# Optimization experiments

Measured on AMD Instinct MI355X. Metric: run time of the kernel, lower is better.

Reference implementation:

```python
import jax, jax.numpy as jnp
import numpy as np

NEG_SLOPE = 0.2  # PyG GATConv default negative_slope


def gat_conv(x, src, dst, W, a_src, a_dst, b, N):
    """Single PyG-style GATConv (add_self_loops already applied via src/dst).
    x: [N, F_in], W: [F_in, H*C], a_src/a_dst: [H, C], b: [H*C].
    Returns [N, H*C] (concat=True)."""
    H, C = a_src.shape
    h = (x @ W).reshape(N, H, C)                      # [N,H,C]
    alpha_src = jnp.sum(h * a_src[None], axis=-1)      # [N,H]
    alpha_dst = jnp.sum(h * a_dst[None], axis=-1)      # [N,H]
    e = jax.nn.leaky_relu(alpha_src[src] + alpha_dst[dst], NEG_SLOPE)  # [E,H]
    # numerically stable segment softmax over incoming edges of each dst node
    m = jax.ops.segment_max(e, dst, num_segments=N)    # [N,H]
    m = jnp.where(jnp.isfinite(m), m, 0.0)
    ex = jnp.exp(e - m[dst])                           # [E,H]
    den = jax.ops.segment_sum(ex, dst, num_segments=N) # [N,H]
    alpha = ex / (den[dst] + 1e-16)                    # [E,H]
    out = jax.ops.segment_sum(h[src] * alpha[..., None], dst, num_segments=N)  # [N,H,C]
    return out.reshape(N, H * C) + b


def setup_inputs() -> dict:
    key = jax.random.key(0)
    ks = jax.random.split(key, 9)
    B, N, E = 2, 50000, 800000
    d_model, n_hidden, en_dim, H = 128, 128, 64, 1
    fea_mats = jax.random.normal(ks[0], (B, N, d_model), dtype=jnp.float32)
    edge_index = jax.random.randint(ks[1], (B, 2, E), 0, N, dtype=jnp.int32)
    s1 = 1.0 / np.sqrt(d_model)
    s2 = 1.0 / np.sqrt(n_hidden)
    return {
        "fea_mats": fea_mats,
        "edge_index": edge_index,
        "W1": jax.random.normal(ks[2], (d_model, H * n_hidden), dtype=jnp.float32) * s1,
        "att_src1": jax.random.normal(ks[3], (H, n_hidden), dtype=jnp.float32) * s2,
        "att_dst1": jax.random.normal(ks[4], (H, n_hidden), dtype=jnp.float32) * s2,
        "b1": jnp.zeros((H * n_hidden,), dtype=jnp.float32),
        "W2": jax.random.normal(ks[5], (H * n_hidden, H * en_dim), dtype=jnp.float32) * s2,
        "att_src2": jax.random.normal(ks[6], (H, en_dim), dtype=jnp.float32) / np.sqrt(en_dim),
        "att_dst2": jax.random.normal(ks[7], (H, en_dim), dtype=jnp.float32) / np.sqrt(en_dim),
        "b2": jnp.zeros((H * en_dim,), dtype=jnp.float32),
    }


def reference(fea_mats, edge_index, W1, att_src1, att_dst1, b1, W2, att_src2, att_dst2, b2):
    B, N, _ = fea_mats.shape
    loops = jnp.arange(N, dtype=edge_index.dtype)

    def per_graph(x, ei):
        # PyG GATConv adds self-loops by default
        src = jnp.concatenate([ei[0], loops])
        dst = jnp.concatenate([ei[1], loops])
        h = gat_conv(x, src, dst, W1, att_src1, att_dst1, b1, N)
        h = jax.nn.relu(h)
        h = gat_conv(h, src, dst, W2, att_src2, att_dst2, b2, N)
        return h  # [N, en_dim]

    return jax.vmap(per_graph)(fea_mats, edge_index)  # [B, N, en_dim]
```

## Files before the change

kernel.cpp:

```cpp
#include <hip/hip_runtime.h>

#define NEG_SLOPE 0.2f
static constexpr int BLK = 256;
static constexpr int EPB = 4096;
static constexpr int CAP = 6144;

typedef short bf16x8 __attribute__((ext_vector_type(8)));
typedef float f32x4  __attribute__((ext_vector_type(4)));
typedef unsigned short u16x8 __attribute__((ext_vector_type(8)));
typedef unsigned short u16x4 __attribute__((ext_vector_type(4)));

static inline int cdiv(long a, long b){ return (int)((a + b - 1) / b); }

__device__ __forceinline__ unsigned short f2bf(float f){
    unsigned u = __float_as_uint(f);
    u += 0x7fff + ((u >> 16) & 1);
    return (unsigned short)(u >> 16);
}
__device__ __forceinline__ float bf2f(unsigned short h){
    return __uint_as_float(((unsigned)h) << 16);
}
__device__ __forceinline__ float lrelu(float v){
    return v > 0.f ? v : NEG_SLOPE * v;
}

struct GP {
    const int* src; const int* dst; const float* X;
    int* gcnt; int* gbase; int* ebuf; int* rowptr; int* csrsrc;
    unsigned short* h1b; unsigned short* h2b;
    float *as1, *ad1, *as2, *ad2; float* outp;
};

template<int CO, int CT, bool RELU_IN, bool BF16OUT>
__device__ __forceinline__ void gemm_dev(
    int bid, const float* __restrict__ X,
    const unsigned short* __restrict__ Wt_hi, const unsigned short* __restrict__ Wt_lo,
    const float* __restrict__ avs, const float* __restrict__ avd,
    void* __restrict__ Hout, float* __restrict__ as_out, float* __restrict__ ad_out,
    int N, unsigned short* smem)
{
    constexpr int CHUNKS = CO / (CT * 16);
    constexpr int HWB = CT * 4096;
    int ch, rtb;
    if (CHUNKS == 1){ ch = 0; rtb = bid; } else { ch = bid & 1; rtb = bid >> 1; }
    int c0 = ch * (CT * 16);

    {
        const char* srch = (const char*)(Wt_hi + (size_t)c0 * 128);
        const char* srcl = (const char*)(Wt_lo + (size_t)c0 * 128);
        #pragma unroll
        for (int it = 0; it < CT * 2; ++it){
            int o = (it * 256 + (int)threadIdx.x) * 16;
            const char* sp = (o < HWB) ? (srch + o) : (srcl + (o - HWB));
            u16x8 v = *(const u16x8*)sp;
            int so = o ^ (((o >> 8) & 7) << 4);
            *(u16x8*)((char*)smem + so) = v;
        }
    }
    __syncthreads();

    int wave = threadIdx.x >> 6;
    int lane = threadIdx.x & 63;
    int RTt = N >> 4;
    int rt0 = rtb * 8 + wave;
    int rt1 = rt0 + 4;
    if (rt0 >= RTt) return;
    bool vB = rt1 < RTt;
    int rl = lane & 15, g = lane >> 4;
    const float* xrowA = X + (long)(rt0 * 16 + rl) * 128 + g * 8;
    const float* xrowB = X + (long)((vB ? rt1 : rt0) * 16 + rl) * 128 + g * 8;

    f32x4 accA[CT], accB[CT];
    #pragma unroll
    for (int t = 0; t < CT; t++){ accA[t] = (f32x4)(0.f); accB[t] = (f32x4)(0.f); }

    int sw = (rl & 7) << 4;
    #pragma unroll
    for (int ks = 0; ks < 4; ks++){
        float4 xaA = *(const float4*)(xrowA + ks * 32);
        float4 xbA = *(const float4*)(xrowA + ks * 32 + 4);
        float4 xaB = *(const float4*)(xrowB + ks * 32);
        float4 xbB = *(const float4*)(xrowB + ks * 32 + 4);
        float xvA[8] = {xaA.x, xaA.y, xaA.z, xaA.w, xbA.x, xbA.y, xbA.z, xbA.w};
        float xvB[8] = {xaB.x, xaB.y, xaB.z, xaB.w, xbB.x, xbB.y, xbB.z, xbB.w};
        bf16x8 xbfA, xbfB;
        #pragma unroll
        for (int j = 0; j < 8; j++){
            float xA = xvA[j], xB = xvB[j];
            if (RELU_IN){ xA = fmaxf(xA, 0.f); xB = fmaxf(xB, 0.f); }
            xbfA[j] = (short)f2bf(xA);
            xbfB[j] = (short)f2bf(xB);
        }
        int rbase = rl * 256 + ks * 64 + g * 16;
        #pragma unroll
        for (int t = 0; t < CT; t++){
            bf16x8 wh = *(const bf16x8*)((char*)smem + ((t * 4096 + rbase) ^ sw));
            bf16x8 wl = *(const bf16x8*)((char*)smem + ((HWB + t * 4096 + rbase) ^ sw));
            accA[t] = __builtin_amdgcn_mfma_f32_16x16x32_bf16(wh, xbfA, accA[t], 0, 0, 0);
            accB[t] = __builtin_amdgcn_mfma_f32_16x16x32_bf16(wh, xbfB, accB[t], 0, 0, 0);
            accA[t] = __builtin_amdgcn_mfma_f32_16x16x32_bf16(wl, xbfA, accA[t], 0, 0, 0);
            accB[t] = __builtin_amdgcn_mfma_f32_16x16x32_bf16(wl, xbfB, accB[t], 0, 0, 0);
        }
    }

    #pragma unroll
    for (int half = 0; half < 2; half++){
        if (half == 1 && !vB) break;
        int r0 = (half == 0 ? rt0 : rt1) << 4;
        f32x4* acc = (half == 0) ? accA : accB;
        float ps = 0.f, pd = 0.f;
        #pragma unroll
        for (int t = 0; t < CT; t++){
            int c = c0 + t * 16 + 4 * g;
            float4 vs4 = *(const float4*)(avs + c);
            float4 vd4 = *(const float4*)(avd + c);
            ps += acc[t][0]*vs4.x + acc[t][1]*vs4.y + acc[t][2]*vs4.z + acc[t][3]*vs4.w;
            pd += acc[t][0]*vd4.x + acc[t][1]*vd4.y + acc[t][2]*vd4.z + acc[t][3]*vd4.w;
            long base = (long)(r0 + rl) * CO + c;
            if (BF16OUT){
                u16x4 pk;
                #pragma unroll
                for (int r = 0; r < 4; r++) pk[r] = f2bf(acc[t][r]);
                *(u16x4*)((unsigned short*)Hout + base) = pk;
            } else {
                float4 pv;
                pv.x = acc[t][0]; pv.y = acc[t][1]; pv.z = acc[t][2]; pv.w = acc[t][3];
                *(float4*)((float*)Hout + base) = pv;
            }
        }
        ps += __shfl_xor(ps, 16, 64); ps += __shfl_xor(ps, 32, 64);
        pd += __shfl_xor(pd, 16, 64); pd += __shfl_xor(pd, 32, 64);
        if (g == 0){
            unsafeAtomicAdd(as_out + r0 + rl, ps);
            unsafeAtomicAdd(ad_out + r0 + rl, pd);
        }
    }
}

__device__ __forceinline__ void bucket_dev(
    int bid, const GP* __restrict__ g, int E, int Etot, int nbk, unsigned short* smem)
{
    int* spk   = (int*)smem;
    int* shist = spk + 4096;
    int* sbase = shist + 256;
    int tid = (int)threadIdx.x;
    for (int i = tid; i < nbk; i += 256) shist[i] = 0;
    __syncthreads();
    int e0 = bid * EPB;
    #pragma unroll
    for (int i = 0; i < EPB / 256; i++){
        int idx = i * 256 + tid; int e = e0 + idx;
        unsigned p = 0xFFFFFFFFu;
        if (e < Etot){
            int s, d;
            if (e < E){ s = g->src[e]; d = g->dst[e]; } else { s = e - E; d = s; }
            p = ((unsigned)s << 16) | (unsigned)d;
            atomicAdd(&shist[d >> 8], 1);
        }
        spk[idx] = (int)p;
    }
    __syncthreads();
    for (int i = tid; i < nbk; i += 256){
        sbase[i] = atomicAdd(&g->gcnt[i], shist[i]);
        shist[i] = 0;
    }
    __syncthreads();
    #pragma unroll
    for (int i = 0; i < EPB / 256; i++){
        int idx = i * 256 + tid;
        unsigned p = (unsigned)spk[idx];
        if (p != 0xFFFFFFFFu){
            int d = (int)(p & 0xFFFFu); int b = d >> 8;
            int r = sbase[b] + atomicAdd(&shist[b], 1);
            if (r < CAP) g->ebuf[(size_t)b * CAP + r] = (int)p;
        }
    }
}

__device__ __forceinline__ void fine_dev(int k, const GP* __restrict__ g, int N, int Etot)
{
    __shared__ int pk2[CAP];
    __shared__ int fs[256];
    __shared__ int fill[256];
    __shared__ int fh[256];
    int tid = (int)threadIdx.x;
    int cnt = min(g->gcnt[k], CAP);
    int bb  = g->gbase[k];
    for (int i = tid; i < cnt; i += 256) pk2[i] = g->ebuf[(size_t)k * CAP + i];
    fh[tid] = 0; fill[tid] = 0;
    __syncthreads();
    for (int i = tid; i < cnt; i += 256) atomicAdd(&fh[pk2[i] & 255], 1);
    __syncthreads();
    int v = fh[tid];
    fs[tid] = v;
    __syncthreads();
    #pragma unroll
    for (int off = 1; off < 256; off <<= 1){
        int t = (tid >= off) ? fs[tid - off] : 0;
        __syncthreads();
        fs[tid] += t;
        __syncthreads();
    }
    int excl = fs[tid] - v;
    __syncthreads();
    fs[tid] = excl;
    __syncthreads();
    int node = k * 256 + tid;
    if (node < N) g->rowptr[node] = bb + excl;
    if (k == 0 && tid == 0) g->rowptr[N] = Etot;
    for (int i = tid; i < cnt; i += 256){
        unsigned p = (unsigned)pk2[i];
        int f = (int)(p & 255u);
        int r = atomicAdd(&fill[f], 1);
        g->csrsrc[bb + fs[f] + r] = (int)(p >> 16);
    }
}

template<int CO, int GRP>
__device__ __forceinline__ void agg_core(
    const int* __restrict__ rowptr, const int* __restrict__ csr_src,
    const float* __restrict__ as, const float* __restrict__ ad,
    const unsigned short* __restrict__ hb, int node, int ql, float* acc)
{
    int start = rowptr[node];
    int deg   = rowptr[node + 1] - start;
    float adv = ad[node];

    int sv[4]; float ev[4];
    #pragma unroll
    for (int q = 0; q < 4; q++){
        int idx = q * GRP + ql;
        sv[q] = 0; ev[q] = -1e30f;
        if (idx < deg){ sv[q] = csr_src[start + idx]; ev[q] = lrelu(as[sv[q]] + adv); }
    }
    float m = fmaxf(fmaxf(ev[0], ev[1]), fmaxf(ev[2], ev[3]));
    if (deg > 4 * GRP){
        for (int j = 4 * GRP + ql; j < deg; j += GRP)
            m = fmaxf(m, lrelu(as[csr_src[start + j]] + adv));
    }
    #pragma unroll
    for (int off = GRP >> 1; off; off >>= 1) m = fmaxf(m, __shfl_xor(m, off, GRP));

    float xq[4]; float sum = 0.f;
    #pragma unroll
    for (int q = 0; q < 4; q++){
        xq[q] = (q * GRP + ql < deg) ? __expf(ev[q] - m) : 0.f;
        sum += xq[q];
    }
    if (deg > 4 * GRP){
        for (int j = 4 * GRP + ql; j < deg; j += GRP)
            sum += __expf(lrelu(as[csr_src[start + j]] + adv) - m);
    }
    #pragma unroll
    for (int off = GRP >> 1; off; off >>= 1) sum += __shfl_xor(sum, off, GRP);
    float inv = 1.f / (sum + 1e-16f);

    #pragma unroll
    for (int i = 0; i < 8; i++) acc[i] = 0.f;

    #pragma unroll
    for (int q = 0; q < 4; q++){
        int rem = deg - q * GRP;
        if (rem <= 0) break;
        int lim = rem < GRP ? rem : GRP;
        float aq = xq[q] * inv; int sq = sv[q];
        int t = 0;
        for (; t + 3 < lim; t += 4){
            int   s0 = __shfl(sq, t+0, GRP), s1 = __shfl(sq, t+1, GRP);
            int   s2 = __shfl(sq, t+2, GRP), s3 = __shfl(sq, t+3, GRP);
            float a0 = __shfl(aq, t+0, GRP), a1 = __shfl(aq, t+1, GRP);
            float a2 = __shfl(aq, t+2, GRP), a3 = __shfl(aq, t+3, GRP);
            u16x8 r0 = *(const u16x8*)(hb + (long)s0 * CO + ql * 8);
            u16x8 r1 = *(const u16x8*)(hb + (long)s1 * CO + ql * 8);
            u16x8 r2 = *(const u16x8*)(hb + (long)s2 * CO + ql * 8);
            u16x8 r3 = *(const u16x8*)(hb + (long)s3 * CO + ql * 8);
            #pragma unroll
            for (int i = 0; i < 8; i++)
                acc[i] += a0 * bf2f(r0[i]) + a1 * bf2f(r1[i])
                        + a2 * bf2f(r2[i]) + a3 * bf2f(r3[i]);
        }
        for (; t < lim; t++){
            int   s0 = __shfl(sq, t, GRP);
            float a0 = __shfl(aq, t, GRP);
            u16x8 r0 = *(const u16x8*)(hb + (long)s0 * CO + ql * 8);
            #pragma unroll
            for (int i = 0; i < 8; i++) acc[i] += a0 * bf2f(r0[i]);
        }
        if (lim < GRP) break;
    }
    if (deg > 4 * GRP){
        for (int j = 4 * GRP; j < deg; j++){
            int sj = csr_src[start + j];
            float aj = __expf(lrelu(as[sj] + adv) - m) * inv;
            u16x8 r0 = *(const u16x8*)(hb + (long)sj * CO + ql * 8);
            #pragma unroll
            for (int i = 0; i < 8; i++) acc[i] += aj * bf2f(r0[i]);
        }
    }
}

__global__ __launch_bounds__(BLK) void prep_k(
    const float* __restrict__ W1, const float* __restrict__ W2,
    unsigned short* __restrict__ w1h, unsigned short* __restrict__ w1l,
    unsigned short* __restrict__ w2h, unsigned short* __restrict__ w2l)
{
    int i = blockIdx.x * BLK + threadIdx.x;
    if (i < 128 * 128){
        int c = i >> 7, k = i & 127;
        float w = W1[k * 128 + c];
        unsigned short hi = f2bf(w);
        w1h[i] = hi; w1l[i] = f2bf(w - bf2f(hi));
        if (i < 64 * 128){
            float w2 = W2[k * 64 + c];
            unsigned short hi2 = f2bf(w2);
            w2h[i] = hi2; w2l[i] = f2bf(w2 - bf2f(hi2));
        }
    }
}

__global__ __launch_bounds__(256, 4) void kA(
    GP a, GP b, const unsigned short* __restrict__ w1h, const unsigned short* __restrict__ w1l,
    const float* __restrict__ avs1, const float* __restrict__ avd1,
    int EB_a, int EB_b, int GB_a, int GB_b, int E, int Etot, int N, int nbk)
{
    __shared__ unsigned short smem[16384];
    int bid = blockIdx.x;
    if (bid < EB_a){ bucket_dev(bid, &a, E, Etot, nbk, smem); return; }
    bid -= EB_a;
    if (bid < EB_b){ bucket_dev(bid, &b, E, Etot, nbk, smem); return; }
    bid -= EB_b;
    if (bid < GB_a){ gemm_dev<128,4,false,true>(bid, a.X, w1h, w1l, avs1, avd1, a.h1b, a.as1, a.ad1, N, smem); return; }
    bid -= GB_a;
    if (bid < GB_b) gemm_dev<128,4,false,true>(bid, b.X, w1h, w1l, avs1, avd1, b.h1b, b.as1, b.ad1, N, smem);
}

__global__ __launch_bounds__(256) void kscan(GP a, GP b, int nbk){
    const GP* g = (blockIdx.x == 0) ? &a : &b;
    __shared__ int sh[256];
    int tid = (int)threadIdx.x;
    int v = (tid < nbk) ? g->gcnt[tid] : 0;
    sh[tid] = v;
    __syncthreads();
    #pragma unroll
    for (int off = 1; off < 256; off <<= 1){
        int t = (tid >= off) ? sh[tid - off] : 0;
        __syncthreads();
        sh[tid] += t;
        __syncthreads();
    }
    if (tid < nbk) g->gbase[tid] = sh[tid] - v;
}

__global__ __launch_bounds__(256) void kB(GP a, GP b, int nb_a, int nb_b, int N, int Etot){
    int bid = blockIdx.x; const GP* g; int k;
    if (bid < nb_a){ g = &a; k = bid; }
    else { k = bid - nb_a; if (k >= nb_b) return; g = &b; }
    fine_dev(k, g, N, Etot);
}

__global__ __launch_bounds__(BLK) void agg1f_k(
    GP a, GP b, const float* __restrict__ b1,
    const unsigned short* __restrict__ w2h, const unsigned short* __restrict__ w2l,
    const float* __restrict__ avs2, const float* __restrict__ avd2,
    int AB_a, int AB_b, int N)
{
    __shared__ unsigned short xlds[32 * 128];
    int bid = blockIdx.x; const GP* g;
    if (bid < AB_a){ g = &a; }
    else { bid -= AB_a; if (bid >= AB_b) return; g = &b; }
    int tid = (int)threadIdx.x;
    int grp = tid >> 4, ql = tid & 15;

    #pragma unroll
    for (int h = 0; h < 2; h++){
        int node = bid * 32 + h * 16 + grp;
        u16x8 xv;
        if (node < N){
            float acc[8];
            agg_core<128,16>(g->rowptr, g->csrsrc, g->as1, g->ad1, g->h1b, node, ql, acc);
            #pragma unroll
            for (int i = 0; i < 8; i++)
                xv[i] = f2bf(fmaxf(acc[i] + b1[ql * 8 + i], 0.f));
        } else {
            #pragma unroll
            for (int i = 0; i < 8; i++) xv[i] = 0;
        }
        int row = h * 16 + grp;
        int bo = (row * 256 + ql * 16) ^ ((row & 7) << 4);
        *(u16x8*)((char*)xlds + bo) = xv;
    }
    __syncthreads();

    int lane = tid & 63, wv = tid >> 6;
    int rl = lane & 15, kg = lane >> 4;
    float pvs = avs2[wv * 16 + rl], pvd = avd2[wv * 16 + rl];
    #pragma unroll
    for (int h = 0; h < 2; h++){
        f32x4 d = (f32x4)(0.f);
        #pragma unroll
        for (int kb = 0; kb < 4; kb++){
            int row = h * 16 + rl;
            bf16x8 af = *(const bf16x8*)((char*)xlds + ((row * 256 + kb * 64 + kg * 16) ^ ((row & 7) << 4)));
            long wo = (long)(wv * 16 + rl) * 128 + kb * 32 + kg * 8;
            bf16x8 bh = *(const bf16x8*)(w2h + wo);
            bf16x8 bl = *(const bf16x8*)(w2l + wo);
            d = __builtin_amdgcn_mfma_f32_16x16x32_bf16(af, bh, d, 0, 0, 0);
            d = __builtin_amdgcn_mfma_f32_16x16x32_bf16(af, bl, d, 0, 0, 0);
        }
        #pragma unroll
        for (int reg = 0; reg < 4; reg++){
            int nd = bid * 32 + h * 16 + 4 * kg + reg;
            float hv = d[reg];
            if (nd < N) g->h2b[(long)nd * 64 + wv * 16 + rl] = f2bf(hv);
            float s_ = hv * pvs, d_ = hv * pvd;
            #pragma unroll
            for (int off = 1; off < 16; off <<= 1){
                s_ += __shfl_xor(s_, off, 16);
                d_ += __shfl_xor(d_, off, 16);
            }
            if (rl == 0 && nd < N){
                unsafeAtomicAdd(g->as2 + nd, s_);
                unsafeAtomicAdd(g->ad2 + nd, d_);
            }
        }
    }
}

__global__ __launch_bounds__(BLK) void agg2f_k(
    GP a, GP b, const float* __restrict__ bias, int AB_a, int AB_b, int N)
{
    int bid = blockIdx.x; const GP* g;
    if (bid < AB_a){ g = &a; }
    else { bid -= AB_a; if (bid >= AB_b) return; g = &b; }
    int tid = (int)threadIdx.x;
    int grp = tid >> 3, ql = tid & 7;
    int node = bid * 32 + grp;
    if (node >= N) return;
    float acc[8];
    agg_core<64,8>(g->rowptr, g->csrsrc, g->as2, g->ad2, g->h2b, node, ql, acc);
    float* o = g->outp + (long)node * 64 + ql * 8;
    #pragma unroll
    for (int i = 0; i < 8; i += 4){
        float4 ov;
        ov.x = acc[i+0] + bias[ql * 8 + i + 0];
        ov.y = acc[i+1] + bias[ql * 8 + i + 1];
        ov.z = acc[i+2] + bias[ql * 8 + i + 2];
        ov.w = acc[i+3] + bias[ql * 8 + i + 3];
        *(float4*)(o + i) = ov;
    }
}

extern "C" void kernel_launch(void* const* d_in, const int* in_sizes, int n_in,
                              void* d_out, int out_size, void* d_ws, size_t ws_size,
                              hipStream_t stream)
{
    const float* fea  = (const float*)d_in[0];
    const int*   ei   = (const int*)  d_in[1];
    const float* W1   = (const float*)d_in[2];
    const float* av_s1= (const float*)d_in[3];
    const float* av_d1= (const float*)d_in[4];
    const float* b1   = (const float*)d_in[5];
    const float* W2   = (const float*)d_in[6];
    const float* av_s2= (const float*)d_in[7];
    const float* av_d2= (const float*)d_in[8];
    const float* b2   = (const float*)d_in[9];
    float* out = (float*)d_out;

    const int B = 2;
    const int N = out_size / (B * 64);
    const int E = in_sizes[1] / (2 * B);
    const int Etot = E + N;
    const int nbk = (N + 255) >> 8;

    size_t pg = 256 + (size_t)nbk * CAP + (size_t)(N + 2) + (size_t)Etot
              + (size_t)N * (64 + 32);
    size_t wtf = 8192 + 8192 + 4096 + 4096;
    auto total_f = [&](int ng){ return wtf + (size_t)ng * (4 * (size_t)N + 256) + (size_t)ng * pg + 64; };
    bool fused = (ws_size >= total_f(2) * sizeof(float));
    int NG = fused ? 2 : 1;

    float* ws = (float*)d_ws;
    size_t off = 0;
    unsigned short* w1h = (unsigned short*)(ws + off); off += 8192;
    unsigned short* w1l = (unsigned short*)(ws + off); off += 8192;
    unsigned short* w2h = (unsigned short*)(ws + off); off += 4096;
    unsigned short* w2l = (unsigned short*)(ws + off); off += 4096;

    float* zbase = ws + off;
    size_t znum = (size_t)NG * (4 * (size_t)N + 256);
    off += znum;

    GP g[2];
    for (int gi = 0; gi < NG; gi++){
        GP p;
        p.as1  = zbase + (size_t)gi * (4 * (size_t)N + 256);
        p.ad1  = p.as1 + N;
        p.as2  = p.ad1 + N;
        p.ad2  = p.as2 + N;
        p.gcnt = (int*)(p.ad2 + N);
        p.gbase  = (int*)(ws + off); off += 256;
        p.ebuf   = (int*)(ws + off); off += (size_t)nbk * CAP;
        p.rowptr = (int*)(ws + off); off += (size_t)(N + 2);
        p.csrsrc = (int*)(ws + off); off += Etot;
        p.h1b  = (unsigned short*)(ws + off); off += (size_t)N * 64;
        p.h2b  = (unsigned short*)(ws + off); off += (size_t)N * 32;
        g[gi] = p;
    }

    const int RT  = N >> 4;
    const int GB1 = cdiv(RT, 8) * 2;
    const int EBk = cdiv(Etot, EPB);
    const int AB1 = cdiv(N, 32);
    const int AB2 = cdiv(N, 32);

    if (fused){
        for (int bi = 0; bi < 2; bi++){
            g[bi].src = ei + (size_t)bi * 2 * E;
            g[bi].dst = g[bi].src + E;
            g[bi].X   = fea + (size_t)bi * N * 128;
            g[bi].outp= out + (size_t)bi * N * 64;
        }
        hipMemsetAsync(zbase, 0, znum * sizeof(float), stream);
        prep_k<<<cdiv(128*128, BLK), BLK, 0, stream>>>(W1, W2, w1h, w1l, w2h, w2l);
        kA<<<2*EBk + 2*GB1, 256, 0, stream>>>(g[0], g[1], w1h, w1l, av_s1, av_d1,
                                              EBk, EBk, GB1, GB1, E, Etot, N, nbk);
        kscan<<<2, 256, 0, stream>>>(g[0], g[1], nbk);
        kB<<<2*nbk, 256, 0, stream>>>(g[0], g[1], nbk, nbk, N, Etot);
        agg1f_k<<<2*AB1, BLK, 0, stream>>>(g[0], g[1], b1, w2h, w2l, av_s2, av_d2, AB1, AB1, N);
        agg2f_k<<<2*AB2, BLK, 0, stream>>>(g[0], g[1], b2, AB2, AB2, N);
    } else {
        prep_k<<<cdiv(128*128, BLK), BLK, 0, stream>>>(W1, W2, w1h, w1l, w2h, w2l);
        for (int bi = 0; bi < B; bi++){
            GP p = g[0];
            p.src = ei + (size_t)bi * 2 * E;
            p.dst = p.src + E;
            p.X   = fea + (size_t)bi * N * 128;
            p.outp= out + (size_t)bi * N * 64;
            hipMemsetAsync(zbase, 0, znum * sizeof(float), stream);
            kA<<<EBk + GB1, 256, 0, stream>>>(p, p, w1h, w1l, av_s1, av_d1,
                                              EBk, 0, GB1, 0, E, Etot, N, nbk);
            kscan<<<1, 256, 0, stream>>>(p, p, nbk);
            kB<<<nbk, 256, 0, stream>>>(p, p, nbk, 0, N, Etot);
            agg1f_k<<<AB1, BLK, 0, stream>>>(p, p, b1, w2h, w2l, av_s2, av_d2, AB1, 0, N);
            agg2f_k<<<AB2, BLK, 0, stream>>>(p, p, b2, AB2, 0, N);
        }
    }
}
```

Before: 202.9 us.

## Make agg1f per-wave: each wave owns 16 nodes and all output columns

Restructures the fused layer-1 aggregation plus layer-2 projection so each wave aggregates 16 nodes into its own LDS slice and then computes all 64 output columns for those nodes. This drops the block-wide __syncthreads and replaces the per-row atomic adds to as2/ad2 with direct stores, since one wave now owns the full dot product for each node. Blocks now cover 64 nodes instead of 32, which halves the grid, and each wave holds four accumulator tiles. The trade is more registers per thread and extra global weight loads per wave.

Measured after the change: 217.9 us. 7.4% more time.

```diff
diff --git a/kernel.cpp b/kernel.cpp
--- a/kernel.cpp
+++ b/kernel.cpp
@@ -364,64 +364,75 @@
     const float* __restrict__ avs2, const float* __restrict__ avd2,
     int AB_a, int AB_b, int N)
 {
-    __shared__ unsigned short xlds[32 * 128];
+    __shared__ unsigned short xlds[4][16 * 128];
     int bid = blockIdx.x; const GP* g;
     if (bid < AB_a){ g = &a; }
     else { bid -= AB_a; if (bid >= AB_b) return; g = &b; }
     int tid = (int)threadIdx.x;
-    int grp = tid >> 4, ql = tid & 15;
-
-    #pragma unroll
-    for (int h = 0; h < 2; h++){
-        int node = bid * 32 + h * 16 + grp;
+    int wv = tid >> 6, lane = tid & 63;
+    int kg = lane >> 4, rl = lane & 15;
+    int wbase = bid * 64 + wv * 16;
+    unsigned short* wlds = &xlds[wv][0];
+
+    #pragma unroll
+    for (int p = 0; p < 4; p++){
+        int row = p * 4 + kg;
+        int node = wbase + row;
         u16x8 xv;
         if (node < N){
             float acc[8];
-            agg_core<128,16>(g->rowptr, g->csrsrc, g->as1, g->ad1, g->h1b, node, ql, acc);
+            agg_core<128,16>(g->rowptr, g->csrsrc, g->as1, g->ad1, g->h1b, node, rl, acc);
             #pragma unroll
             for (int i = 0; i < 8; i++)
-                xv[i] = f2bf(fmaxf(acc[i] + b1[ql * 8 + i], 0.f));
+                xv[i] = f2bf(fmaxf(acc[i] + b1[rl * 8 + i], 0.f));
         } else {
             #pragma unroll
             for (int i = 0; i < 8; i++) xv[i] = 0;
         }
-        int row = h * 16 + grp;
-        int bo = (row * 256 + ql * 16) ^ ((row & 7) << 4);
-        *(u16x8*)((char*)xlds + bo) = xv;
-    }
-    __syncthreads();
-
-    int lane = tid & 63, wv = tid >> 6;
-    int rl = lane & 15, kg = lane >> 4;
-    float pvs = avs2[wv * 16 + rl], pvd = avd2[wv * 16 + rl];
-    #pragma unroll
-    for (int h = 0; h < 2; h++){
-        f32x4 d = (f32x4)(0.f);
-        #pragma unroll
-        for (int kb = 0; kb < 4; kb++){
-            int row = h * 16 + rl;
-            bf16x8 af = *(const bf16x8*)((char*)xlds + ((row * 256 + kb * 64 + kg * 16) ^ ((row & 7) << 4)));
-            long wo = (long)(wv * 16 + rl) * 128 + kb * 32 + kg * 8;
+        int bo = (row * 256 + rl * 16) ^ ((row & 7) << 4);
+        *(u16x8*)((char*)wlds + bo) = xv;
+    }
+
+    f32x4 d[4];
+    #pragma unroll
+    for (int t = 0; t < 4; t++) d[t] = (f32x4)(0.f);
+    #pragma unroll
+    for (int kb = 0; kb < 4; kb++){
+        bf16x8 af = *(const bf16x8*)((char*)wlds + ((rl * 256 + kb * 64 + kg * 16) ^ ((rl & 7) << 4)));
+        #pragma unroll
+        for (int t = 0; t < 4; t++){
+            long wo = (long)(t * 16 + rl) * 128 + kb * 32 + kg * 8;
             bf16x8 bh = *(const bf16x8*)(w2h + wo);
             bf16x8 bl = *(const bf16x8*)(w2l + wo);
-            d = __builtin_amdgcn_mfma_f32_16x16x32_bf16(af, bh, d, 0, 0, 0);
-            d = __builtin_amdgcn_mfma_f32_16x16x32_bf16(af, bl, d, 0, 0, 0);
-        }
+            d[t] = __builtin_amdgcn_mfma_f32_16x16x32_bf16(af, bh, d[t], 0, 0, 0);
+            d[t] = __builtin_amdgcn_mfma_f32_16x16x32_bf16(af, bl, d[t], 0, 0, 0);
+        }
+    }
+
+    float sreg[4] = {0.f, 0.f, 0.f, 0.f}, dreg[4] = {0.f, 0.f, 0.f, 0.f};
+    #pragma unroll
+    for (int t = 0; t < 4; t++){
+        float vs = avs2[t * 16 + rl], vd = avd2[t * 16 + rl];
         #pragma unroll
         for (int reg = 0; reg < 4; reg++){
-            int nd = bid * 32 + h * 16 + 4 * kg + reg;
-            float hv = d[reg];
-            if (nd < N) g->h2b[(long)nd * 64 + wv * 16 + rl] = f2bf(hv);
-            float s_ = hv * pvs, d_ = hv * pvd;
-            #pragma unroll
-            for (int off = 1; off < 16; off <<= 1){
-                s_ += __shfl_xor(s_, off, 16);
-                d_ += __shfl_xor(d_, off, 16);
-            }
-            if (rl == 0 && nd < N){
-                unsafeAtomicAdd(g->as2 + nd, s_);
-                unsafeAtomicAdd(g->ad2 + nd, d_);
-            }
+            float hv = d[t][reg];
+            int nd = wbase + 4 * kg + reg;
+            if (nd < N) g->h2b[(long)nd * 64 + t * 16 + rl] = f2bf(hv);
+            sreg[reg] += hv * vs;
+            dreg[reg] += hv * vd;
+        }
+    }
+    #pragma unroll
+    for (int reg = 0; reg < 4; reg++){
+        #pragma unroll
+        for (int off = 1; off < 16; off <<= 1){
+            sreg[reg] += __shfl_xor(sreg[reg], off, 16);
+            dreg[reg] += __shfl_xor(dreg[reg], off, 16);
+        }
+        int nd = wbase + 4 * kg + reg;
+        if (rl == 0 && nd < N){
+            g->as2[nd] = sreg[reg];
+            g->ad2[nd] = dreg[reg];
         }
     }
 }
@@ -510,7 +521,7 @@
     const int RT  = N >> 4;
     const int GB1 = cdiv(RT, 8) * 2;
     const int EBk = cdiv(Etot, EPB);
-    const int AB1 = cdiv(N, 32);
+    const int AB1 = cdiv(N, 64);
     const int AB2 = cdiv(N, 32);
 
     if (fused){
```

## Skew layer aggregations across graphs to overlap layer-1 and layer-2 work

Applied to the files above, without the earlier changes.

Layer-1 and layer-2 aggregation are merged into one mixed kernel whose blocks are split by an interleaved ratio between graph-1 layer-1 work and graph-0 layer-2 work. The launches are staggered: graph 0 layer 1, then graph 1 layer 1 alongside graph 0 layer 2, then graph 1 layer 2. Layer-1 blocks now handle 16 nodes instead of 32, which halves LDS use and doubles the block count. The intent is to fill the GPU with mixed workloads and to shorten the tail of each phase, at the cost of one extra launch and more per-block fixed overhead.

Measured after the change: 226.7 us. 11.7% more time.

```diff
diff --git a/kernel.cpp b/kernel.cpp
--- a/kernel.cpp
+++ b/kernel.cpp
@@ -299,6 +299,85 @@
     }
 }
 
+__device__ __forceinline__ void agg1_dev(
+    int bid, const GP* __restrict__ g, const float* __restrict__ b1,
+    const unsigned short* __restrict__ w2h, const unsigned short* __restrict__ w2l,
+    const float* __restrict__ avs2, const float* __restrict__ avd2,
+    int N, unsigned short* xlds)
+{
+    int tid = (int)threadIdx.x;
+    int grp = tid >> 4, ql = tid & 15;
+    int node = bid * 16 + grp;
+
+    {
+        u16x8 xv;
+        if (node < N){
+            float acc[8];
+            agg_core<128,16>(g->rowptr, g->csrsrc, g->as1, g->ad1, g->h1b, node, ql, acc);
+            #pragma unroll
+            for (int i = 0; i < 8; i++)
+                xv[i] = f2bf(fmaxf(acc[i] + b1[ql * 8 + i], 0.f));
+        } else {
+            #pragma unroll
+            for (int i = 0; i < 8; i++) xv[i] = 0;
+        }
+        int bo = (grp * 256 + ql * 16) ^ ((grp & 7) << 4);
+        *(u16x8*)((char*)xlds + bo) = xv;
+    }
+    __syncthreads();
+
+    int lane = tid & 63, wv = tid >> 6;
+    int rl = lane & 15, kg = lane >> 4;
+    f32x4 d = (f32x4)(0.f);
+    #pragma unroll
+    for (int kb = 0; kb < 4; kb++){
+        bf16x8 af = *(const bf16x8*)((char*)xlds + ((rl * 256 + kb * 64 + kg * 16) ^ ((rl & 7) << 4)));
+        long wo = (long)(wv * 16 + rl) * 128 + kb * 32 + kg * 8;
+        bf16x8 bh = *(const bf16x8*)(w2h + wo);
+        bf16x8 bl = *(const bf16x8*)(w2l + wo);
+        d = __builtin_amdgcn_mfma_f32_16x16x32_bf16(af, bh, d, 0, 0, 0);
+        d = __builtin_amdgcn_mfma_f32_16x16x32_bf16(af, bl, d, 0, 0, 0);
+    }
+    float pvs = avs2[wv * 16 + rl], pvd = avd2[wv * 16 + rl];
+    #pragma unroll
+    for (int reg = 0; reg < 4; reg++){
+        int nd = bid * 16 + 4 * kg + reg;
+        float hv = d[reg];
+        if (nd < N) g->h2b[(long)nd * 64 + wv * 16 + rl] = f2bf(hv);
+        float s_ = hv * pvs, d_ = hv * pvd;
+        #pragma unroll
+        for (int off = 1; off < 16; off <<= 1){
+            s_ += __shfl_xor(s_, off, 16);
+            d_ += __shfl_xor(d_, off, 16);
+        }
+        if (rl == 0 && nd < N){
+            unsafeAtomicAdd(g->as2 + nd, s_);
+            unsafeAtomicAdd(g->ad2 + nd, d_);
+        }
+    }
+}
+
+__device__ __forceinline__ void agg2_dev(
+    int bid, const GP* __restrict__ g, const float* __restrict__ bias, int N)
+{
+    int tid = (int)threadIdx.x;
+    int grp = tid >> 3, ql = tid & 7;
+    int node = bid * 32 + grp;
+    if (node >= N) return;
+    float acc[8];
+    agg_core<64,8>(g->rowptr, g->csrsrc, g->as2, g->ad2, g->h2b, node, ql, acc);
+    float* o = g->outp + (long)node * 64 + ql * 8;
+    #pragma unroll
+    for (int i = 0; i < 8; i += 4){
+        float4 ov;
+        ov.x = acc[i+0] + bias[ql * 8 + i + 0];
+        ov.y = acc[i+1] + bias[ql * 8 + i + 1];
+        ov.z = acc[i+2] + bias[ql * 8 + i + 2];
+        ov.w = acc[i+3] + bias[ql * 8 + i + 3];
+        *(float4*)(o + i) = ov;
+    }
+}
+
 __global__ __launch_bounds__(BLK) void prep_k(
     const float* __restrict__ W1, const float* __restrict__ W2,
     unsigned short* __restrict__ w1h, unsigned short* __restrict__ w1l,
@@ -358,95 +437,22 @@
     fine_dev(k, g, N, Etot);
 }
 
-__global__ __launch_bounds__(BLK) void agg1f_k(
-    GP a, GP b, const float* __restrict__ b1,
+__global__ __launch_bounds__(BLK) void aggmix_k(
+    GP g1, GP g2, const float* __restrict__ b1, const float* __restrict__ b2,
     const unsigned short* __restrict__ w2h, const unsigned short* __restrict__ w2l,
     const float* __restrict__ avs2, const float* __restrict__ avd2,
-    int AB_a, int AB_b, int N)
-{
-    __shared__ unsigned short xlds[32 * 128];
-    int bid = blockIdx.x; const GP* g;
-    if (bid < AB_a){ g = &a; }
-    else { bid -= AB_a; if (bid >= AB_b) return; g = &b; }
-    int tid = (int)threadIdx.x;
-    int grp = tid >> 4, ql = tid & 15;
-
-    #pragma unroll
-    for (int h = 0; h < 2; h++){
-        int node = bid * 32 + h * 16 + grp;
-        u16x8 xv;
-        if (node < N){
-            float acc[8];
-            agg_core<128,16>(g->rowptr, g->csrsrc, g->as1, g->ad1, g->h1b, node, ql, acc);
-            #pragma unroll
-            for (int i = 0; i < 8; i++)
-                xv[i] = f2bf(fmaxf(acc[i] + b1[ql * 8 + i], 0.f));
-        } else {
-            #pragma unroll
-            for (int i = 0; i < 8; i++) xv[i] = 0;
-        }
-        int row = h * 16 + grp;
-        int bo = (row * 256 + ql * 16) ^ ((row & 7) << 4);
-        *(u16x8*)((char*)xlds + bo) = xv;
-    }
-    __syncthreads();
-
-    int lane = tid & 63, wv = tid >> 6;
-    int rl = lane & 15, kg = lane >> 4;
-    float pvs = avs2[wv * 16 + rl], pvd = avd2[wv * 16 + rl];
-    #pragma unroll
-    for (int h = 0; h < 2; h++){
-        f32x4 d = (f32x4)(0.f);
-        #pragma unroll
-        for (int kb = 0; kb < 4; kb++){
-            int row = h * 16 + rl;
-            bf16x8 af = *(const bf16x8*)((char*)xlds + ((row * 256 + kb * 64 + kg * 16) ^ ((row & 7) << 4)));
-            long wo = (long)(wv * 16 + rl) * 128 + kb * 32 + kg * 8;
-            bf16x8 bh = *(const bf16x8*)(w2h + wo);
-            bf16x8 bl = *(const bf16x8*)(w2l + wo);
-            d = __builtin_amdgcn_mfma_f32_16x16x32_bf16(af, bh, d, 0, 0, 0);
-            d = __builtin_amdgcn_mfma_f32_16x16x32_bf16(af, bl, d, 0, 0, 0);
-        }
-        #pragma unroll
-        for (int reg = 0; reg < 4; reg++){
-            int nd = bid * 32 + h * 16 + 4 * kg + reg;
-            float hv = d[reg];
-            if (nd < N) g->h2b[(long)nd * 64 + wv * 16 + rl] = f2bf(hv);
-            float s_ = hv * pvs, d_ = hv * pvd;
-            #pragma unroll
-            for (int off = 1; off < 16; off <<= 1){
-                s_ += __shfl_xor(s_, off, 16);
-                d_ += __shfl_xor(d_, off, 16);
-            }
-            if (rl == 0 && nd < N){
-                unsafeAtomicAdd(g->as2 + nd, s_);
-                unsafeAtomicAdd(g->ad2 + nd, d_);
-            }
-        }
-    }
-}
-
-__global__ __launch_bounds__(BLK) void agg2f_k(
-    GP a, GP b, const float* __restrict__ bias, int AB_a, int AB_b, int N)
-{
-    int bid = blockIdx.x; const GP* g;
-    if (bid < AB_a){ g = &a; }
-    else { bid -= AB_a; if (bid >= AB_b) return; g = &b; }
-    int tid = (int)threadIdx.x;
-    int grp = tid >> 3, ql = tid & 7;
-    int node = bid * 32 + grp;
-    if (node >= N) return;
-    float acc[8];
-    agg_core<64,8>(g->rowptr, g->csrsrc, g->as2, g->ad2, g->h2b, node, ql, acc);
-    float* o = g->outp + (long)node * 64 + ql * 8;
-    #pragma unroll
-    for (int i = 0; i < 8; i += 4){
-        float4 ov;
-        ov.x = acc[i+0] + bias[ql * 8 + i + 0];
-        ov.y = acc[i+1] + bias[ql * 8 + i + 1];
-        ov.z = acc[i+2] + bias[ql * 8 + i + 2];
-        ov.w = acc[i+3] + bias[ql * 8 + i + 3];
-        *(float4*)(o + i) = ov;
+    int n1, int n2, int N)
+{
+    __shared__ unsigned short xlds[16 * 128];
+    int bid = blockIdx.x;
+    int T = n1 + n2;
+    long lo  = (long)bid * n1 / T;
+    long hi2 = (long)(bid + 1) * n1 / T;
+    if (hi2 > lo){
+        agg1_dev((int)lo, &g1, b1, w2h, w2l, avs2, avd2, N, xlds);
+    } else {
+        int l = bid - (int)lo;
+        if (l < n2) agg2_dev(l, &g2, b2, N);
     }
 }
 
@@ -510,7 +516,7 @@
     const int RT  = N >> 4;
     const int GB1 = cdiv(RT, 8) * 2;
     const int EBk = cdiv(Etot, EPB);
-    const int AB1 = cdiv(N, 32);
+    const int AB1 = cdiv(N, 16);
     const int AB2 = cdiv(N, 32);
 
     if (fused){
@@ -526,8 +532,9 @@
                                               EBk, EBk, GB1, GB1, E, Etot, N, nbk);
         kscan<<<2, 256, 0, stream>>>(g[0], g[1], nbk);
         kB<<<2*nbk, 256, 0, stream>>>(g[0], g[1], nbk, nbk, N, Etot);
-        agg1f_k<<<2*AB1, BLK, 0, stream>>>(g[0], g[1], b1, w2h, w2l, av_s2, av_d2, AB1, AB1, N);
-        agg2f_k<<<2*AB2, BLK, 0, stream>>>(g[0], g[1], b2, AB2, AB2, N);
+        aggmix_k<<<AB1,       BLK, 0, stream>>>(g[0], g[0], b1, b2, w2h, w2l, av_s2, av_d2, AB1, 0,   N);
+        aggmix_k<<<AB1 + AB2, BLK, 0, stream>>>(g[1], g[0], b1, b2, w2h, w2l, av_s2, av_d2, AB1, AB2, N);
+        aggmix_k<<<AB2,       BLK, 0, stream>>>(g[1], g[1], b1, b2, w2h, w2l, av_s2, av_d2, 0,   AB2, N);
     } else {
         prep_k<<<cdiv(128*128, BLK), BLK, 0, stream>>>(W1, W2, w1h, w1l, w2h, w2l);
         for (int bi = 0; bi < B; bi++){
@@ -541,8 +548,8 @@
                                               EBk, 0, GB1, 0, E, Etot, N, nbk);
             kscan<<<1, 256, 0, stream>>>(p, p, nbk);
             kB<<<nbk, 256, 0, stream>>>(p, p, nbk, 0, N, Etot);
-            agg1f_k<<<AB1, BLK, 0, stream>>>(p, p, b1, w2h, w2l, av_s2, av_d2, AB1, 0, N);
-            agg2f_k<<<AB2, BLK, 0, stream>>>(p, p, b2, AB2, 0, N);
-        }
-    }
-}
+            aggmix_k<<<AB1, BLK, 0, stream>>>(p, p, b1, b2, w2h, w2l, av_s2, av_d2, AB1, 0, N);
+            aggmix_k<<<AB2, BLK, 0, stream>>>(p, p, b1, b2, w2h, w2l, av_s2, av_d2, 0, AB2, N);
+        }
+    }
+}
```
